# Performance work log

Measured on AMD Instinct MI355X. Metric: run time of the kernel, lower is better.

Reference implementation:

```python
import jax, jax.numpy as jnp
import numpy as np

WS = 8        # window_size
NH = 16       # num_heads
EPS = 1e-5    # BatchNorm eps (inference mode: running_mean=0, running_var=1)

def conv2d(x, w, padding=0, groups=1):
    return jax.lax.conv_general_dilated(
        x, w, (1, 1), [(padding, padding), (padding, padding)],
        dimension_numbers=('NCHW', 'OIHW', 'NCHW'), feature_group_count=groups)

def bn(x, gamma, beta):
    # eval-mode BatchNorm with running_mean=0, running_var=1
    return x * (gamma / jnp.sqrt(1.0 + EPS))[None, :, None, None] + beta[None, :, None, None]

def avgpool(x, kh, kw, ph, pw):
    # torch AvgPool2d with count_include_pad=True: sum over zero-padded window / (kh*kw)
    s = jax.lax.reduce_window(x, 0.0, jax.lax.add, (1, 1, kh, kw), (1, 1, 1, 1),
                              [(0, 0), (0, 0), (ph, ph), (pw, pw)])
    return s / float(kh * kw)

def rel_pos_index(ws):
    coords = np.stack(np.meshgrid(np.arange(ws), np.arange(ws), indexing='ij')).reshape(2, -1)
    rel = (coords[:, :, None] - coords[:, None, :]).transpose(1, 2, 0) + (ws - 1)
    return (rel[..., 0] * (2 * ws - 1) + rel[..., 1]).reshape(-1)

def hge_kernels(W):
    # build 4 directional Sobel kernels + Gaussian-Laplacian from learned scalars
    S0, S45, S90 = W[:, :, 0, 0], W[:, :, 0, 1], W[:, :, 0, 2]
    S135, GL = W[:, :, 1, 0], W[:, :, 2, 2]
    z = jnp.zeros_like(S0)
    k3 = lambda rows: jnp.stack([jnp.stack(r, -1) for r in rows], -2)  # [O,I,3,3]
    w0 = k3([[S0, 2*S0, S0], [z, z, z], [-S0, -2*S0, -S0]])
    w45 = k3([[2*S45, S45, z], [S45, z, -S45], [z, -S45, -2*S45]])
    w90 = k3([[S90, z, -S90], [2*S90, z, -2*S90], [S90, z, -S90]])
    w135 = k3([[z, -S135, -2*S135], [S135, z, -S135], [2*S135, S135, z]])
    a1 = GL * 4.0; a2 = -a1 / 8.0; a3 = -a1 / 16.0
    wGL = jnp.zeros(S0.shape + (5, 5), S0.dtype)
    for i, j, v in [(0,2,a3),(1,1,a3),(1,2,a2),(1,3,a3),(2,0,a3),(2,1,a2),(2,2,a1),
                    (2,3,a2),(2,4,a3),(3,1,a3),(3,2,a2),(3,3,a3),(4,2,a3)]:
        wGL = wGL.at[:, :, i, j].set(v)
    return w0, w45, w90, w135, wGL

def forward(x, ca_h1, ca_w1, ca_fh, ca_fw, l1_w, l1_g, l1_b, l2_w, l2_g, l2_b,
            hge_w, hge_fc_w, hge_fc_b, qkv_w, rel_table, proj_dw, proj_g, proj_b, proj_pw):
    B, C, H, W = x.shape
    d = C // NH
    scale = d ** -0.5
    # --- CA block: coordinate attention (1x1 convs on H- and W-pooled features) ---
    cm = lambda w, t: jnp.einsum('oc,bc...->bo...', w, t)
    s_h = jax.nn.sigmoid(cm(ca_fh, cm(ca_h1, x.mean(3))))   # [B,C,H]
    s_w = jax.nn.sigmoid(cm(ca_fw, cm(ca_w1, x.mean(2))))   # [B,C,W]
    x = x * s_h[:, :, :, None] * s_w[:, :, None, :]
    # --- local branch: 1x1 ConvBN + 3x3 ConvBN + HGE edge operator ---
    local = bn(conv2d(x, l2_w), l2_g, l2_b) + bn(conv2d(x, l1_w, padding=1), l1_g, l1_b)
    w0, w45, w90, w135, wGL = hge_kernels(hge_w)
    feats = jnp.concatenate([conv2d(x, w0, 1), conv2d(x, w45, 1), conv2d(x, w90, 1),
                             conv2d(x, w135, 1), conv2d(x, wGL, 2)], axis=1)  # [B,5C,H,W]
    local = local + conv2d(feats, hge_fc_w) + hge_fc_b[None, :, None, None]
    # --- windowed attention ---
    ph, pw = (-H) % WS, (-W) % WS
    if ph or pw:
        x = jnp.pad(x, ((0, 0), (0, 0), (0, ph), (0, pw)), mode='reflect')
    Hp, Wp = x.shape[2], x.shape[3]
    hh, ww = Hp // WS, Wp // WS
    qkv = conv2d(x, qkv_w)                                   # [B,3C,Hp,Wp]
    qkv = qkv.reshape(B, 3, NH, d, hh, WS, ww, WS)
    qkv = qkv.transpose(1, 0, 4, 6, 2, 5, 7, 3).reshape(3, B * hh * ww, NH, WS * WS, d)
    q, k, v = qkv[0], qkv[1], qkv[2]
    bias = rel_table[rel_pos_index(WS)].reshape(WS * WS, WS * WS, NH).transpose(2, 0, 1)
    dots = jnp.einsum('wnid,wnjd->wnij', q, k) * scale + bias[None]
    attn = jax.nn.softmax(dots, axis=-1)
    o = jnp.einsum('wnij,wnjd->wnid', attn, v)
    o = o.reshape(B, hh, ww, NH, WS, WS, d).transpose(0, 3, 6, 1, 4, 2, 5)
    o = o.reshape(B, C, Hp, Wp)[:, :, :H, :W]
    # --- directional average pooling of attention output ---
    ox = avgpool(jnp.pad(o, ((0, 0), (0, 0), (0, 1), (0, 0)), mode='reflect'), WS, 1, WS // 2 - 1, 0)
    oy = avgpool(jnp.pad(o, ((0, 0), (0, 0), (0, 0), (0, 1)), mode='reflect'), 1, WS, 0, WS // 2 - 1)
    out = ox + oy + local
    # --- pad_out + separable ConvBN projection (depthwise k=ws -> BN -> 1x1) ---
    out = jnp.pad(out, ((0, 0), (0, 0), (0, 1), (0, 1)), mode='reflect')
    out = conv2d(out, proj_dw, padding=(WS - 1) // 2, groups=C)
    out = bn(out, proj_g, proj_b)
    out = conv2d(out, proj_pw)
    return out[:, :, :H, :W]

def setup_inputs() -> dict:
    key = jax.random.key(0)
    ks = jax.random.split(key, 20)
    C = 128
    f32 = jnp.float32
    n = lambda k, sh, s: jax.random.normal(k, sh, f32) * s
    return {
        'x': jax.random.normal(ks[0], (2, C, 256, 256), f32),
        'ca_h1': n(ks[1], (C, C), 0.05), 'ca_w1': n(ks[2], (C, C), 0.05),
        'ca_fh': n(ks[3], (C, C), 0.05), 'ca_fw': n(ks[4], (C, C), 0.05),
        'l1_w': n(ks[5], (C, C, 3, 3), 0.03),
        'l1_g': 1.0 + n(ks[6], (C,), 0.02), 'l1_b': n(ks[7], (C,), 0.02),
        'l2_w': n(ks[8], (C, C, 1, 1), 0.09),
        'l2_g': 1.0 + n(ks[9], (C,), 0.02), 'l2_b': n(ks[10], (C,), 0.02),
        'hge_w': n(ks[11], (C, C, 3, 3), 0.02),
        'hge_fc_w': n(ks[12], (C, 5 * C, 1, 1), 0.02), 'hge_fc_b': n(ks[13], (C,), 0.02),
        'qkv_w': n(ks[14], (3 * C, C, 1, 1), 0.05),
        'rel_table': n(ks[15], ((2 * WS - 1) ** 2, NH), 0.02),
        'proj_dw': n(ks[16], (C, 1, WS, WS), 0.05),
        'proj_g': 1.0 + n(ks[17], (C,), 0.02), 'proj_b': n(ks[18], (C,), 0.02),
        'proj_pw': n(ks[19], (C, C, 1, 1), 0.05),
    }

def reference(x, ca_h1, ca_w1, ca_fh, ca_fw, l1_w, l1_g, l1_b, l2_w, l2_g, l2_b,
              hge_w, hge_fc_w, hge_fc_b, qkv_w, rel_table, proj_dw, proj_g, proj_b, proj_pw):
    return forward(x, ca_h1, ca_w1, ca_fh, ca_fw, l1_w, l1_g, l1_b, l2_w, l2_g, l2_b,
                   hge_w, hge_fc_w, hge_fc_b, qkv_w, rel_table, proj_dw, proj_g, proj_b, proj_pw)
```

## Files before the change

kernel.cpp:

```cpp
#include <hip/hip_runtime.h>

#define BB 2
#define CC 128
#define HWSZ 65536
#define RSQE 0.9999950000374997f
#define ATT_SCALE 0.35355339059327373f

typedef unsigned short u16;
using short8 = __attribute__((ext_vector_type(8))) short;
using f32x4  = __attribute__((ext_vector_type(4))) float;

#if defined(__has_builtin)
# if __has_builtin(__builtin_amdgcn_fdot2_f32_bf16)
#  define HAVE_DOT2 1
# endif
#endif

__device__ __forceinline__ float b2f(u16 u){
  return __uint_as_float(((unsigned int)u) << 16);
}
__device__ __forceinline__ u16 f2b(float f){
  unsigned int v = __float_as_uint(f);
  unsigned int r = (v + 0x7FFFu + ((v >> 16) & 1u)) >> 16;
  return (u16)r;
}

__device__ const int c_DI[13] = {-2,-1,-1,-1, 0, 0,0,0,0, 1,1,1, 2};
__device__ const int c_DJ[13] = { 0,-1, 0, 1,-2,-1,0,1,2,-1,0,1, 0};

__global__ void k_detect(const u16* __restrict__ xr, int* __restrict__ flag){
  __shared__ int ws_[4];
  int tid = threadIdx.x;
  int cnt = 0;
  for (int i = 0; i < 16; ++i){
    u16 u = xr[tid*16 + i];
    int e = (u >> 7) & 0xFF;
    cnt += (e < 100 || e > 141) ? 1 : 0;
  }
  #pragma unroll
  for (int off = 32; off > 0; off >>= 1) cnt += __shfl_down(cnt, off, 64);
  if ((tid & 63) == 0) ws_[tid >> 6] = cnt;
  __syncthreads();
  if (tid == 0) *flag = (ws_[0]+ws_[1]+ws_[2]+ws_[3] > 64) ? 1 : 0;
}

__global__ void k_ingest4(const void* __restrict__ src, u16* __restrict__ dst,
                          int n4, const int* __restrict__ flag){
  int i = blockIdx.x * 256 + threadIdx.x;
  if (i >= n4) return;
  if (*flag){
    float4 f = ((const float4*)src)[i];
    ushort4 r; r.x=f2b(f.x); r.y=f2b(f.y); r.z=f2b(f.z); r.w=f2b(f.w);
    ((ushort4*)dst)[i] = r;
  } else {
    ((ushort4*)dst)[i] = ((const ushort4*)src)[i];
  }
}

struct PtrL { const void* p[19]; };

__global__ void k_ingest_w(PtrL pl, u16* __restrict__ dst, const int* __restrict__ flag){
  const int ends[19] = {16384,32768,49152,65536,212992,213120,213248,229632,229760,
                        229888,377344,459264,459392,508544,512144,520336,520464,520592,536976};
  int g = blockIdx.x * 256 + threadIdx.x;
  int idx = g * 4;
  if (idx >= 536976) return;
  int seg = 0, start = 0;
  #pragma unroll
  for (int s = 0; s < 19; ++s){ if (idx >= ends[s]){ seg = s+1; start = ends[s]; } }
  int local = idx - start;
  const void* sp = pl.p[seg];
  if (*flag){
    float4 f = ((const float4*)sp)[local >> 2];
    ushort4 r; r.x=f2b(f.x); r.y=f2b(f.y); r.z=f2b(f.z); r.w=f2b(f.w);
    *(ushort4*)(dst + idx) = r;
  } else {
    *(ushort4*)(dst + idx) = ((const ushort4*)sp)[local >> 2];
  }
}

__global__ void k_prep_A(const u16* __restrict__ fh, const u16* __restrict__ h1,
                         const u16* __restrict__ fw, const u16* __restrict__ w1,
                         const u16* __restrict__ l1b, const u16* __restrict__ l2b,
                         const u16* __restrict__ fcb,
                         float* __restrict__ A_h, float* __restrict__ A_w,
                         float* __restrict__ biasK){
  int idx = blockIdx.x * 256 + threadIdx.x;
  int o = idx >> 7, c = idx & 127;
  float ah = 0.f, aw = 0.f;
  for (int m = 0; m < 128; ++m){
    ah += b2f(fh[o*128 + m]) * b2f(h1[m*128 + c]);
    aw += b2f(fw[o*128 + m]) * b2f(w1[m*128 + c]);
  }
  A_h[idx] = ah; A_w[idx] = aw;
  if (c == 0) biasK[o] = b2f(l1b[o]) + b2f(l2b[o]) + b2f(fcb[o]);
}

__global__ void k_prep_rel(const u16* __restrict__ rel, float* __restrict__ relo){
  int idx = blockIdx.x * 256 + threadIdx.x;
  if (idx >= 3600) return;
  int head = idx / 225, i = idx - head*225;
  relo[idx] = b2f(rel[i*16 + head]);
}

__global__ void k_prep_K(const u16* __restrict__ hge_w, const u16* __restrict__ fc_w,
                         const u16* __restrict__ l1_w, const u16* __restrict__ l1_g,
                         const u16* __restrict__ l2_w, const u16* __restrict__ l2_g,
                         u16* __restrict__ Kwb){
  int idx = blockIdx.x * 256 + threadIdx.x;
  int o = idx >> 7, c = idx & 127;
  float m0=0.f, m45=0.f, m90=0.f, m135=0.f, mgl=0.f;
  const u16* fo = fc_w + o*640;
  for (int m = 0; m < 128; ++m){
    const u16* hw9 = hge_w + (size_t)(m*128 + c)*9;
    m0   += b2f(fo[m      ]) * b2f(hw9[0]);
    m45  += b2f(fo[128 + m]) * b2f(hw9[1]);
    m90  += b2f(fo[256 + m]) * b2f(hw9[2]);
    m135 += b2f(fo[384 + m]) * b2f(hw9[3]);
    mgl  += b2f(fo[512 + m]) * b2f(hw9[8]);
  }
  float g1 = b2f(l1_g[o]) * RSQE;
  float g2 = b2f(l2_g[o]) * RSQE;
  float l1v[9];
  #pragma unroll
  for (int t = 0; t < 9; ++t) l1v[t] = b2f(l1_w[(size_t)idx*9 + t]) * g1;
  float l2v = b2f(l2_w[idx]) * g2;
  float kp[13];
  kp[0]  = -0.25f*mgl;
  kp[1]  =  m0 + 2.f*m45 + m90              - 0.25f*mgl + l1v[0];
  kp[2]  =  2.f*m0 + m45 - m135             - 0.50f*mgl + l1v[1];
  kp[3]  =  m0 - m90 - 2.f*m135             - 0.25f*mgl + l1v[2];
  kp[4]  = -0.25f*mgl;
  kp[5]  =  m45 + 2.f*m90 + m135            - 0.50f*mgl + l1v[3];
  kp[6]  =  4.f*mgl + l1v[4] + l2v;
  kp[7]  = -m45 - 2.f*m90 - m135            - 0.50f*mgl + l1v[5];
  kp[8]  = -0.25f*mgl;
  kp[9]  = -m0 + m90 + 2.f*m135             - 0.25f*mgl + l1v[6];
  kp[10] = -2.f*m0 - m45 + m135             - 0.50f*mgl + l1v[7];
  kp[11] = -m0 - 2.f*m45 - m90              - 0.25f*mgl + l1v[8];
  kp[12] = -0.25f*mgl;
  #pragma unroll
  for (int t = 0; t < 13; ++t) Kwb[t*16384 + idx] = f2b(kp[t]);
}

__global__ void k_means(const u16* __restrict__ x, float* __restrict__ mh, float* __restrict__ mw){
  __shared__ float colpart[4][256];
  int c = blockIdx.x, b = blockIdx.y;
  const u16* xp = x + (size_t)(b*CC + c)*HWSZ;
  int tid = threadIdx.x, lane = tid & 63, wv = tid >> 6;
  float c0=0.f,c1=0.f,c2=0.f,c3=0.f;
  for (int r = 0; r < 64; ++r){
    int h = wv*64 + r;
    ushort4 u = *(const ushort4*)(xp + h*256 + lane*4);
    float v0=b2f(u.x), v1=b2f(u.y), v2=b2f(u.z), v3=b2f(u.w);
    c0+=v0; c1+=v1; c2+=v2; c3+=v3;
    float rs = v0+v1+v2+v3;
    #pragma unroll
    for (int off = 32; off > 0; off >>= 1) rs += __shfl_down(rs, off, 64);
    if (lane == 0) mh[(size_t)(b*CC + c)*256 + h] = rs * (1.0f/256.0f);
  }
  colpart[wv][lane*4+0]=c0; colpart[wv][lane*4+1]=c1;
  colpart[wv][lane*4+2]=c2; colpart[wv][lane*4+3]=c3;
  __syncthreads();
  mw[(size_t)(b*CC + c)*256 + tid] =
    (colpart[0][tid]+colpart[1][tid]+colpart[2][tid]+colpart[3][tid]) * (1.0f/256.0f);
}

__global__ void k_sig(const float* __restrict__ A_h, const float* __restrict__ A_w,
                      const float* __restrict__ mh, const float* __restrict__ mw,
                      float* __restrict__ s_h, float* __restrict__ s_w){
  int o = blockIdx.x, b = blockIdx.y, sel = blockIdx.z, t = threadIdx.x;
  const float* A = sel ? A_w : A_h;
  const float* m = sel ? mw : mh;
  float* s = sel ? s_w : s_h;
  float acc = 0.f;
  for (int c = 0; c < 128; ++c)
    acc += A[o*128 + c] * m[(size_t)(b*CC + c)*256 + t];
  s[(size_t)(b*CC + o)*256 + t] = 1.0f / (1.0f + __expf(-acc));
}

__global__ void k_scale2cl(const u16* __restrict__ cx, const float* __restrict__ s_h,
                           const float* __restrict__ s_w, u16* __restrict__ xcl){
  __shared__ u16 t[16][136];
  int b = blockIdx.z >> 8, h = blockIdx.z & 255;
  int w0 = blockIdx.x * 16;
  int tid = threadIdx.x;
  int ic = tid >> 1, wseg = (tid & 1) * 8;
  uint4 v = *(const uint4*)(cx + (size_t)(b*CC + ic)*HWSZ + h*256 + w0 + wseg);
  float sh = s_h[(size_t)(b*CC + ic)*256 + h];
  const float* swp = s_w + (size_t)(b*CC + ic)*256 + w0 + wseg;
  float4 swa = *(const float4*)swp;
  float4 swb = *(const float4*)(swp + 4);
  u16 tmp[8]; *(uint4*)tmp = v;
  t[wseg+0][ic] = f2b(b2f(tmp[0])*sh*swa.x);
  t[wseg+1][ic] = f2b(b2f(tmp[1])*sh*swa.y);
  t[wseg+2][ic] = f2b(b2f(tmp[2])*sh*swa.z);
  t[wseg+3][ic] = f2b(b2f(tmp[3])*sh*swa.w);
  t[wseg+4][ic] = f2b(b2f(tmp[4])*sh*swb.x);
  t[wseg+5][ic] = f2b(b2f(tmp[5])*sh*swb.y);
  t[wseg+6][ic] = f2b(b2f(tmp[6])*sh*swb.z);
  t[wseg+7][ic] = f2b(b2f(tmp[7])*sh*swb.w);
  __syncthreads();
  int w = tid >> 4, part = (tid & 15) * 8;
  uint4 o = *(const uint4*)&t[w][part];
  *(uint4*)(xcl + ((size_t)(b*256 + h)*256 + (w0 + w))*128 + part) = o;
}

__global__ void k_cf2cl(const u16* __restrict__ src, u16* __restrict__ dst){
  __shared__ u16 t[16][136];
  int b = blockIdx.z >> 8, h = blockIdx.z & 255;
  int w0 = blockIdx.x * 16;
  int tid = threadIdx.x;
  int ic = tid >> 1, wseg = (tid & 1) * 8;
  uint4 v = *(const uint4*)(src + (size_t)(b*CC + ic)*HWSZ + h*256 + w0 + wseg);
  u16 tmp[8]; *(uint4*)tmp = v;
  #pragma unroll
  for (int k = 0; k < 8; ++k) t[wseg + k][ic] = tmp[k];
  __syncthreads();
  int w = tid >> 4, part = (tid & 15) * 8;
  uint4 o = *(const uint4*)&t[w][part];
  *(uint4*)(dst + ((size_t)(b*256 + h)*256 + (w0 + w))*128 + part) = o;
}

__launch_bounds__(256)
__global__ void k_conv5m(const u16* __restrict__ xcl, const u16* __restrict__ Kwb,
                         const float* __restrict__ biasK, u16* __restrict__ outp){
  __shared__ u16 As[128][40];
  __shared__ u16 Bs[128][40];
  int tid = threadIdx.x;
  int wv = tid >> 6, lane = tid & 63;
  int q = lane >> 4, l16 = lane & 15;
  int pt = blockIdx.x;
  int b = pt >> 9, h = (pt >> 1) & 255, w0 = (pt & 1) << 7;
  int mrow = (wv & 1) << 6, nrow = (wv >> 1) << 6;
  int sr = tid >> 2, sp = (tid & 3) << 3;
  const u16* xb_b = xcl + (size_t)b*HWSZ*128;
  f32x4 acc[4][4];
  #pragma unroll
  for (int mt = 0; mt < 4; ++mt)
    #pragma unroll
    for (int nt = 0; nt < 4; ++nt) acc[mt][nt] = (f32x4){0.f,0.f,0.f,0.f};

  for (int kc = 0; kc < 52; ++kc){
    int t = kc >> 2, c0 = (kc & 3) << 5;
    int di = c_DI[t], dj = c_DJ[t];
    int hh2 = h + di;
    bool rowok = (unsigned)hh2 < 256u;
    const u16* rowp = xb_b + (size_t)(rowok ? hh2 : 0)*256*128 + c0 + sp;
    int col0 = w0 + dj + sr;
    int col1 = col0 + 64;
    __syncthreads();
    {
      uint4 va0 = {0,0,0,0}, va1 = {0,0,0,0};
      if (rowok && (unsigned)col0 < 256u) va0 = *(const uint4*)(rowp + col0*128);
      if (rowok && (unsigned)col1 < 256u) va1 = *(const uint4*)(rowp + col1*128);
      *(uint4*)&As[sr][sp] = va0;
      *(uint4*)&As[sr + 64][sp] = va1;
      const u16* Bb = Kwb + t*16384 + c0;
      *(uint4*)&Bs[sr][sp] = *(const uint4*)(Bb + sr*128 + sp);
      *(uint4*)&Bs[sr + 64][sp] = *(const uint4*)(Bb + (sr + 64)*128 + sp);
    }
    __syncthreads();
    short8 af[4], bf[4];
    #pragma unroll
    for (int mt = 0; mt < 4; ++mt) af[mt] = *(const short8*)&As[mrow + mt*16 + l16][q*8];
    #pragma unroll
    for (int nt = 0; nt < 4; ++nt) bf[nt] = *(const short8*)&Bs[nrow + nt*16 + l16][q*8];
    #pragma unroll
    for (int mt = 0; mt < 4; ++mt)
      #pragma unroll
      for (int nt = 0; nt < 4; ++nt)
        acc[mt][nt] = __builtin_amdgcn_mfma_f32_16x16x32_bf16(af[mt], bf[nt], acc[mt][nt], 0, 0, 0);
  }
  #pragma unroll
  for (int nt = 0; nt < 4; ++nt){
    int n = nrow + nt*16 + l16;
    float bv = biasK[n];
    size_t cbase = (size_t)(b*CC + n)*HWSZ + h*256 + w0;
    #pragma unroll
    for (int mt = 0; mt < 4; ++mt){
      int m = mrow + mt*16 + q*4;
      ushort4 st;
      st.x = f2b(acc[mt][nt][0] + bv);
      st.y = f2b(acc[mt][nt][1] + bv);
      st.z = f2b(acc[mt][nt][2] + bv);
      st.w = f2b(acc[mt][nt][3] + bv);
      *(ushort4*)(outp + cbase + m) = st;
    }
  }
}

__launch_bounds__(256)
__global__ void k_mgemm(const u16* __restrict__ Xcl, const u16* __restrict__ W,
                        u16* __restrict__ Y, float* __restrict__ Yf,
                        const int* __restrict__ flag, int nsel, int mode){
  __shared__ u16 As[128][136];
  __shared__ u16 Bs[128][136];
  int tid = threadIdx.x;
  int wv = tid >> 6, lane = tid & 63;
  int q = lane >> 4, l16 = lane & 15;
  int pt = blockIdx.x;
  int b = pt >> 9, h = (pt >> 1) & 255, w0 = (pt & 1) << 7;
  int mrow = (wv & 1) << 6, nrow = (wv >> 1) << 6;
  const u16* Abase = Xcl + ((size_t)(b*256 + h)*256 + w0)*128;
  #pragma unroll
  for (int i = 0; i < 8; ++i){
    int seg = i*256 + tid;
    *(uint4*)&As[seg >> 4][(seg & 15) << 3] = *(const uint4*)(Abase + seg*8);
  }
  for (int sel = 0; sel < nsel; ++sel){
    __syncthreads();
    const u16* Wb = W + sel*16384;
    #pragma unroll
    for (int i = 0; i < 8; ++i){
      int seg = i*256 + tid;
      *(uint4*)&Bs[seg >> 4][(seg & 15) << 3] = *(const uint4*)(Wb + seg*8);
    }
    __syncthreads();
    f32x4 acc[4][4];
    #pragma unroll
    for (int mt = 0; mt < 4; ++mt)
      #pragma unroll
      for (int nt = 0; nt < 4; ++nt) acc[mt][nt] = (f32x4){0.f,0.f,0.f,0.f};
    #pragma unroll
    for (int kc = 0; kc < 4; ++kc){
      short8 af[4], bf[4];
      #pragma unroll
      for (int mt = 0; mt < 4; ++mt) af[mt] = *(const short8*)&As[mrow + mt*16 + l16][kc*32 + q*8];
      #pragma unroll
      for (int nt = 0; nt < 4; ++nt) bf[nt] = *(const short8*)&Bs[nrow + nt*16 + l16][kc*32 + q*8];
      #pragma unroll
      for (int mt = 0; mt < 4; ++mt)
        #pragma unroll
        for (int nt = 0; nt < 4; ++nt)
          acc[mt][nt] = __builtin_amdgcn_mfma_f32_16x16x32_bf16(af[mt], bf[nt], acc[mt][nt], 0, 0, 0);
    }
    if (mode == 0){
      __syncthreads();
      #pragma unroll
      for (int mt = 0; mt < 4; ++mt){
        int m0i = mrow + mt*16 + q*4;
        #pragma unroll
        for (int nt = 0; nt < 4; ++nt){
          int n = nrow + nt*16 + l16;
          Bs[m0i+0][n] = f2b(acc[mt][nt][0]);
          Bs[m0i+1][n] = f2b(acc[mt][nt][1]);
          Bs[m0i+2][n] = f2b(acc[mt][nt][2]);
          Bs[m0i+3][n] = f2b(acc[mt][nt][3]);
        }
      }
      __syncthreads();
      int win = tid >> 4, head = tid & 15;
      size_t obase = (((((size_t)b*32 + (h >> 3))*32 + (w0 >> 3) + win)*3 + sel)*16 + head)*512
                     + (size_t)(h & 7)*64;
      #pragma unroll
      for (int pj = 0; pj < 8; ++pj){
        uint4 vv = *(const uint4*)&Bs[win*8 + pj][head*8];
        *(uint4*)(Y + obase + pj*8) = vv;
      }
    } else {
      int f32o = (Yf != nullptr) && (*flag != 0);
      #pragma unroll
      for (int nt = 0; nt < 4; ++nt){
        int n = nrow + nt*16 + l16;
        size_t cbase = (size_t)(b*CC + n)*HWSZ + h*256 + w0;
        #pragma unroll
        for (int mt = 0; mt < 4; ++mt){
          int m = mrow + mt*16 + q*4;
          if (f32o){
            float4 st; st.x=acc[mt][nt][0]; st.y=acc[mt][nt][1];
            st.z=acc[mt][nt][2]; st.w=acc[mt][nt][3];
            *(float4*)(Yf + cbase + m) = st;
          } else {
            ushort4 st;
            st.x = f2b(acc[mt][nt][0]); st.y = f2b(acc[mt][nt][1]);
            st.z = f2b(acc[mt][nt][2]); st.w = f2b(acc[mt][nt][3]);
            *(ushort4*)(Y + cbase + m) = st;
          }
        }
      }
    }
  }
}

__launch_bounds__(256)
__global__ void k_attn3(const u16* __restrict__ qkvw, const float* __restrict__ relo,
                        u16* __restrict__ obuf){
  __shared__ float relf[228];
  __shared__ u16  kls[4][64][8];
  __shared__ float vls[4][64][8];
  int tid = threadIdx.x, wv = tid >> 6, lane = tid & 63;
  int b = blockIdx.z >> 4, head = blockIdx.z & 15;
  int hh = blockIdx.y, ww = blockIdx.x * 4 + wv;

  for (int e = tid; e < 225; e += 256) relf[e] = relo[head*225 + e];

  size_t base = (((size_t)b*32 + hh)*32 + ww)*3*8192 + (size_t)head*512;
  uint4 qv = *(const uint4*)(qkvw + base + lane*8);
  *(uint4*)&kls[wv][lane][0] = *(const uint4*)(qkvw + base + 8192 + lane*8);
  {
    uint4 raw = *(const uint4*)(qkvw + base + 16384 + lane*8);
    u16 tv[8]; *(uint4*)tv = raw;
    float4 lo, hi;
    lo.x=b2f(tv[0]); lo.y=b2f(tv[1]); lo.z=b2f(tv[2]); lo.w=b2f(tv[3]);
    hi.x=b2f(tv[4]); hi.y=b2f(tv[5]); hi.z=b2f(tv[6]); hi.w=b2f(tv[7]);
    *(float4*)&vls[wv][lane][0] = lo;
    *(float4*)&vls[wv][lane][4] = hi;
  }
  __syncthreads();

  int qi = lane >> 3, qj = lane & 7;
  const float* rbase = relf + (qi + 7)*15 + (qj + 7);
  float s[64];
#if HAVE_DOT2
  typedef __bf16 bf2 __attribute__((ext_vector_type(2)));
  bf2 q0 = __builtin_bit_cast(bf2, qv.x), q1 = __builtin_bit_cast(bf2, qv.y);
  bf2 q2 = __builtin_bit_cast(bf2, qv.z), q3 = __builtin_bit_cast(bf2, qv.w);
  #pragma unroll
  for (int kp = 0; kp < 64; ++kp){
    uint4 kv = *(const uint4*)&kls[wv][kp][0];
    float d = __builtin_amdgcn_fdot2_f32_bf16(q3, __builtin_bit_cast(bf2, kv.w), 0.f, false);
    d = __builtin_amdgcn_fdot2_f32_bf16(q2, __builtin_bit_cast(bf2, kv.z), d, false);
    d = __builtin_amdgcn_fdot2_f32_bf16(q1, __builtin_bit_cast(bf2, kv.y), d, false);
    d = __builtin_amdgcn_fdot2_f32_bf16(q0, __builtin_bit_cast(bf2, kv.x), d, false);
    s[kp] = fmaf(d, ATT_SCALE, rbase[-((kp>>3)*15 + (kp&7))]);
  }
#else
  float qf[8];
  { u16 tq[8]; *(uint4*)tq = qv;
    #pragma unroll
    for (int d = 0; d < 8; ++d) qf[d] = b2f(tq[d]); }
  #pragma unroll
  for (int kp = 0; kp < 64; ++kp){
    uint4 kv = *(const uint4*)&kls[wv][kp][0];
    u16 tk[8]; *(uint4*)tk = kv;
    float d = 0.f;
    #pragma unroll
    for (int dd = 0; dd < 8; ++dd) d = fmaf(qf[dd], b2f(tk[dd]), d);
    s[kp] = fmaf(d, ATT_SCALE, rbase[-((kp>>3)*15 + (kp&7))]);
  }
#endif
  float t16[16];
  #pragma unroll
  for (int i = 0; i < 16; ++i)
    t16[i] = fmaxf(fmaxf(s[i], s[i+16]), fmaxf(s[i+32], s[i+48]));
  float mx = t16[0];
  #pragma unroll
  for (int i = 1; i < 16; ++i) mx = fmaxf(mx, t16[i]);
  #pragma unroll
  for (int kp = 0; kp < 64; ++kp) s[kp] = __expf(s[kp] - mx);
  #pragma unroll
  for (int i = 0; i < 16; ++i)
    t16[i] = (s[i] + s[i+16]) + (s[i+32] + s[i+48]);
  float sum = t16[0];
  #pragma unroll
  for (int i = 1; i < 16; ++i) sum += t16[i];
  float inv = 1.0f / sum;
  float ov[8] = {0.f,0.f,0.f,0.f,0.f,0.f,0.f,0.f};
  #pragma unroll
  for (int kp = 0; kp < 64; ++kp){
    float4 va = *(const float4*)&vls[wv][kp][0];
    float4 vb = *(const float4*)&vls[wv][kp][4];
    float pp = s[kp];
    ov[0] = fmaf(pp, va.x, ov[0]); ov[1] = fmaf(pp, va.y, ov[1]);
    ov[2] = fmaf(pp, va.z, ov[2]); ov[3] = fmaf(pp, va.w, ov[3]);
    ov[4] = fmaf(pp, vb.x, ov[4]); ov[5] = fmaf(pp, vb.y, ov[5]);
    ov[6] = fmaf(pp, vb.z, ov[6]); ov[7] = fmaf(pp, vb.w, ov[7]);
  }
  size_t obase = (size_t)(b*CC + head*8)*HWSZ + (size_t)(hh*8 + qi)*256 + ww*8 + qj;
  #pragma unroll
  for (int d = 0; d < 8; ++d)
    obuf[obase + (size_t)d*HWSZ] = f2b(ov[d] * inv);
}

__launch_bounds__(256)
__global__ void k_pool2(const u16* __restrict__ obuf, u16* __restrict__ localb){
  __shared__ u16 t[71][88];
  int bc = blockIdx.z;
  int h0 = blockIdx.y * 64, w0 = blockIdx.x * 64;
  int tid = threadIdx.x;
  const u16* op = obuf + (size_t)bc * HWSZ;

  for (int e = tid; e < 710; e += 256){
    int tr = e / 10, ci = e - tr*10;
    int gt = h0 - 3 + tr;
    if (gt == 256) gt = 254;
    bool rv = (unsigned)gt <= 255u;
    int g0 = w0 - 8 + ci*8;
    uint4 v = {0,0,0,0};
    if (rv){
      if (g0 >= 0 && g0 <= 248){
        v = *(const uint4*)(op + gt*256 + g0);
      } else {
        u16 tmp[8];
        #pragma unroll
        for (int j = 0; j < 8; ++j){
          int g = g0 + j;
          if (g == 256) g = 254;
          tmp[j] = ((unsigned)g <= 255u) ? op[gt*256 + g] : (u16)0;
        }
        v = *(const uint4*)tmp;
      }
    }
    *(uint4*)&t[tr][ci*8] = v;
  }
  __syncthreads();

  int ty = tid >> 4, tx = tid & 15;
  int r0 = ty*4, c0 = tx*4;
  float sxv[4][4];
  #pragma unroll
  for (int c = 0; c < 4; ++c){
    float col[11];
    #pragma unroll
    for (int i = 0; i < 11; ++i) col[i] = b2f(t[r0+i][c0+8+c]);
    float s = ((col[0]+col[1])+(col[2]+col[3]))+((col[4]+col[5])+(col[6]+col[7]));
    sxv[0][c] = s;
    s += col[8]  - col[0]; sxv[1][c] = s;
    s += col[9]  - col[1]; sxv[2][c] = s;
    s += col[10] - col[2]; sxv[3][c] = s;
  }
  #pragma unroll
  for (int r = 0; r < 4; ++r){
    int rr = r0 + r;
    float pre[11];
    #pragma unroll
    for (int j = 0; j < 11; ++j) pre[j] = b2f(t[rr+3][c0+5+j]);
    float sy0 = ((pre[0]+pre[1])+(pre[2]+pre[3]))+((pre[4]+pre[5])+(pre[6]+pre[7]));
    float sy1 = sy0 + pre[8]  - pre[0];
    float sy2 = sy1 + pre[9]  - pre[1];
    float sy3 = sy2 + pre[10] - pre[2];
    size_t base = (size_t)bc*HWSZ + (size_t)(h0+rr)*256 + (w0+c0);
    ushort4 lv = *(const ushort4*)(localb + base);
    ushort4 st;
    st.x = f2b((sxv[r][0]+sy0)*0.125f + b2f(lv.x));
    st.y = f2b((sxv[r][1]+sy1)*0.125f + b2f(lv.y));
    st.z = f2b((sxv[r][2]+sy2)*0.125f + b2f(lv.z));
    st.w = f2b((sxv[r][3]+sy3)*0.125f + b2f(lv.w));
    *(ushort4*)(localb + base) = st;
  }
}

__launch_bounds__(256)
__global__ void k_dw2(const u16* __restrict__ u_, const u16* __restrict__ dww,
                      const u16* __restrict__ g, const u16* __restrict__ bta,
                      u16* __restrict__ dwout){
  __shared__ u16 xt[71][152];
  int c = blockIdx.z & 127, b = blockIdx.z >> 7;
  int h0 = blockIdx.y * 64, w0 = blockIdx.x * 128;
  int tid = threadIdx.x;
  const u16* up = u_ + (size_t)(b*CC + c)*HWSZ;

  for (int e = tid; e < 71*18; e += 256){
    int tr = e / 18, ci = e - tr*18;
    int gt = h0 - 3 + tr;
    if (gt == 256) gt = 254;
    int g0 = w0 - 8 + ci*8;
    uint4 v = {0,0,0,0};
    if ((unsigned)gt <= 255u){
      if (g0 >= 0 && g0 <= 248){
        v = *(const uint4*)(up + gt*256 + g0);
      } else {
        u16 tmp[8];
        #pragma unroll
        for (int j = 0; j < 8; ++j){
          int gw = g0 + j;
          if (gw == 256) gw = 254;
          tmp[j] = ((unsigned)gw <= 255u) ? up[gt*256 + gw] : (u16)0;
        }
        v = *(const uint4*)tmp;
      }
    }
    *(uint4*)&xt[tr][ci*8] = v;
  }

#if HAVE_DOT2
  typedef __bf16 bf2v __attribute__((ext_vector_type(2)));
  unsigned int wp[32];
  {
    const uint4* wsrc = (const uint4*)(dww + c*64);
    #pragma unroll
    for (int t = 0; t < 8; ++t){
      uint4 v = wsrc[t];
      wp[t*4+0]=v.x; wp[t*4+1]=v.y; wp[t*4+2]=v.z; wp[t*4+3]=v.w;
    }
  }
#else
  float wf[64];
  {
    const u16* wsrc = dww + c*64;
    #pragma unroll
    for (int t = 0; t < 64; ++t) wf[t] = b2f(wsrc[t]);
  }
#endif
  __syncthreads();

  int tx = tid & 15, ty = tid >> 4;
  int r0 = ty*4;
  int cb = tx*8;
  float acc[4][8];
  #pragma unroll
  for (int r = 0; r < 4; ++r)
    #pragma unroll
    for (int k = 0; k < 8; ++k) acc[r][k] = 0.f;

  #pragma unroll
  for (int i = 0; i < 11; ++i){
    const u16* rowp = &xt[r0 + i][cb + 4];
    uint2 av = *(const uint2*)(rowp);
    uint4 mv = *(const uint4*)(rowp + 4);
    uint2 zv = *(const uint2*)(rowp + 12);
    unsigned int d0=av.x, d1=av.y, d2=mv.x, d3=mv.y, d4=mv.z, d5=mv.w, d6=zv.x, d7=zv.y;
    unsigned int dd[8] = {d0,d1,d2,d3,d4,d5,d6,d7};
#if HAVE_DOT2
    unsigned int xp[15];
    #pragma unroll
    for (int t = 1; t < 15; ++t)
      xp[t] = (t & 1) ? ((dd[t>>1] >> 16) | (dd[(t>>1)+1] << 16)) : dd[t>>1];
    #pragma unroll
    for (int dr = 0; dr < 4; ++dr){
      int wr = i - dr;
      if (wr >= 0 && wr < 8){
        #pragma unroll
        for (int k = 0; k < 8; ++k){
          float s = acc[dr][k];
          #pragma unroll
          for (int p = 0; p < 4; ++p)
            s = __builtin_amdgcn_fdot2_f32_bf16(
                  __builtin_bit_cast(bf2v, wp[wr*4+p]),
                  __builtin_bit_cast(bf2v, xp[1+k+2*p]), s, false);
          acc[dr][k] = s;
        }
      }
    }
#else
    float xw[16];
    #pragma unroll
    for (int t = 1; t < 16; ++t){
      unsigned int w32 = dd[t>>1];
      xw[t] = __uint_as_float((t & 1) ? (w32 & 0xFFFF0000u) : (w32 << 16));
    }
    #pragma unroll
    for (int dr = 0; dr < 4; ++dr){
      int wr = i - dr;
      if (wr >= 0 && wr < 8){
        #pragma unroll
        for (int k = 0; k < 8; ++k){
          float s = acc[dr][k];
          #pragma unroll
          for (int j = 0; j < 8; ++j)
            s = fmaf(wf[wr*8+j], xw[1+k+j], s);
          acc[dr][k] = s;
        }
      }
    }
#endif
  }

  float scale = b2f(g[c]) * RSQE;
  float bb = b2f(bta[c]);
  size_t obase = (size_t)(b*CC + c)*HWSZ + (size_t)(h0 + r0)*256 + w0 + cb;
  #pragma unroll
  for (int r = 0; r < 4; ++r){
    u16 po[8];
    #pragma unroll
    for (int k = 0; k < 8; ++k) po[k] = f2b(acc[r][k]*scale + bb);
    *(uint4*)(dwout + obase + (size_t)r*256) = *(uint4*)po;
  }
}

extern "C" void kernel_launch(void* const* d_in, const int* in_sizes, int n_in,
                              void* d_out, int out_size, void* d_ws, size_t ws_size,
                              hipStream_t stream) {
  char* p = (char*)d_ws;
  u16* cx     = (u16*)p; p += 33554432;
  u16* xcl    = (u16*)p; p += 33554432;
  u16* qkvb   = (u16*)p; p += 100663296;
  u16* cw     = (u16*)p; p += 1074176;
  float* A_h    = (float*)p; p += 65536;
  float* A_w    = (float*)p; p += 65536;
  u16*  Kwb     = (u16*)p;  p += 425984;
  float* biasK  = (float*)p; p += 1024;
  float* mh     = (float*)p; p += 262144;
  float* mw     = (float*)p; p += 262144;
  float* s_h    = (float*)p; p += 262144;
  float* s_w    = (float*)p; p += 262144;
  int* flag     = (int*)p;   p += 256;
  float* relo   = (float*)p; p += 16384;

  u16* localb = (u16*)d_out;
  u16* qkvw   = qkvb;
  u16* obuf   = cx;
  u16* dwbuf  = qkvb;
  u16* dwcl   = xcl;

  const int O_h1=0, O_w1=16384, O_fh=32768, O_fw=49152, O_l1w=65536, O_l1g=212992,
            O_l1b=213120, O_l2w=213248, O_l2g=229632, O_l2b=229760, O_hge=229888,
            O_fcw=377344, O_fcb=459264, O_qkvw=459392, O_rel=508544, O_dw=512144,
            O_pg=520336, O_pb=520464, O_pw=520592;

  k_detect<<<1, 256, 0, stream>>>((const u16*)d_in[0], flag);
  k_ingest4<<<16384, 256, 0, stream>>>(d_in[0], cx, 4194304, flag);
  PtrL pl;
  for (int i = 0; i < 19; ++i) pl.p[i] = d_in[i+1];
  k_ingest_w<<<525, 256, 0, stream>>>(pl, cw, flag);

  k_prep_A<<<64, 256, 0, stream>>>(cw+O_fh, cw+O_h1, cw+O_fw, cw+O_w1,
                                   cw+O_l1b, cw+O_l2b, cw+O_fcb, A_h, A_w, biasK);
  k_prep_rel<<<15, 256, 0, stream>>>(cw+O_rel, relo);
  k_prep_K<<<64, 256, 0, stream>>>(cw+O_hge, cw+O_fcw, cw+O_l1w, cw+O_l1g,
                                   cw+O_l2w, cw+O_l2g, Kwb);
  k_means<<<dim3(128, 2), 256, 0, stream>>>(cx, mh, mw);
  k_sig<<<dim3(128, 2, 2), 256, 0, stream>>>(A_h, A_w, mh, mw, s_h, s_w);
  k_scale2cl<<<dim3(16, 1, 512), 256, 0, stream>>>(cx, s_h, s_w, xcl);

  k_conv5m<<<1024, 256, 0, stream>>>(xcl, Kwb, biasK, localb);
  k_mgemm<<<1024, 256, 0, stream>>>(xcl, cw+O_qkvw, qkvw, nullptr, flag, 3, 0);
  k_attn3<<<dim3(8, 32, 32), 256, 0, stream>>>(qkvw, relo, obuf);
  k_pool2<<<dim3(4, 4, 256), 256, 0, stream>>>(obuf, localb);
  k_dw2<<<dim3(2, 4, 256), 256, 0, stream>>>(localb, cw+O_dw, cw+O_pg, cw+O_pb, dwbuf);
  k_cf2cl<<<dim3(16, 1, 512), 256, 0, stream>>>(dwbuf, dwcl);
  k_mgemm<<<1024, 256, 0, stream>>>(dwcl, cw+O_pw, (u16*)d_out, (float*)d_out, flag, 1, 1);
}
```

Before: 572.0 us.

## Restructure 5x5 sparse conv to stage one input row per kernel row and reuse across taps

The conv kernel now loads a full halo-padded input row (132 pixels x 128 channels) into shared memory once per kernel row and reuses it for every horizontal tap in that row, instead of restaging the input for each of the 13 taps. Weight fragments are read straight from global memory rather than staged in LDS, and block indices are remapped so that consecutive blocks touch different image rows, which changes cache locality. This cuts global input traffic and the number of barriers, at the cost of uncoalesced global weight loads in the inner loop and more LDS per block, which may lower occupancy.

```diff
diff --git a/kernel.cpp b/kernel.cpp
--- a/kernel.cpp
+++ b/kernel.cpp
@@ -24,9 +24,6 @@
   unsigned int r = (v + 0x7FFFu + ((v >> 16) & 1u)) >> 16;
   return (u16)r;
 }
-
-__device__ const int c_DI[13] = {-2,-1,-1,-1, 0, 0,0,0,0, 1,1,1, 2};
-__device__ const int c_DJ[13] = { 0,-1, 0, 1,-2,-1,0,1,2,-1,0,1, 0};
 
 __global__ void k_detect(const u16* __restrict__ xr, int* __restrict__ flag){
   __shared__ int ws_[4];
@@ -223,17 +220,16 @@
 }
 
 __launch_bounds__(256)
-__global__ void k_conv5m(const u16* __restrict__ xcl, const u16* __restrict__ Kwb,
+__global__ void k_conv5r(const u16* __restrict__ xcl, const u16* __restrict__ Kwb,
                          const float* __restrict__ biasK, u16* __restrict__ outp){
-  __shared__ u16 As[128][40];
-  __shared__ u16 Bs[128][40];
+  __shared__ u16 As[132][136];
   int tid = threadIdx.x;
   int wv = tid >> 6, lane = tid & 63;
   int q = lane >> 4, l16 = lane & 15;
-  int pt = blockIdx.x;
+  int pt0 = blockIdx.x;
+  int pt = (pt0 & 7) * 128 + (pt0 >> 3);
   int b = pt >> 9, h = (pt >> 1) & 255, w0 = (pt & 1) << 7;
   int mrow = (wv & 1) << 6, nrow = (wv >> 1) << 6;
-  int sr = tid >> 2, sp = (tid & 3) << 3;
   const u16* xb_b = xcl + (size_t)b*HWSZ*128;
   f32x4 acc[4][4];
   #pragma unroll
@@ -241,36 +237,47 @@
     #pragma unroll
     for (int nt = 0; nt < 4; ++nt) acc[mt][nt] = (f32x4){0.f,0.f,0.f,0.f};
 
-  for (int kc = 0; kc < 52; ++kc){
-    int t = kc >> 2, c0 = (kc & 3) << 5;
-    int di = c_DI[t], dj = c_DJ[t];
-    int hh2 = h + di;
+  const int rowTap0[5] = {0,1,4,9,12};
+  const int rowNTap[5] = {1,3,5,3,1};
+  const int rowDj0[5]  = {0,-1,-2,-1,0};
+
+  for (int ri = 0; ri < 5; ++ri){
+    int hh2 = h + ri - 2;
     bool rowok = (unsigned)hh2 < 256u;
-    const u16* rowp = xb_b + (size_t)(rowok ? hh2 : 0)*256*128 + c0 + sp;
-    int col0 = w0 + dj + sr;
-    int col1 = col0 + 64;
     __syncthreads();
     {
-      uint4 va0 = {0,0,0,0}, va1 = {0,0,0,0};
-      if (rowok && (unsigned)col0 < 256u) va0 = *(const uint4*)(rowp + col0*128);
-      if (rowok && (unsigned)col1 < 256u) va1 = *(const uint4*)(rowp + col1*128);
-      *(uint4*)&As[sr][sp] = va0;
-      *(uint4*)&As[sr + 64][sp] = va1;
-      const u16* Bb = Kwb + t*16384 + c0;
-      *(uint4*)&Bs[sr][sp] = *(const uint4*)(Bb + sr*128 + sp);
-      *(uint4*)&Bs[sr + 64][sp] = *(const uint4*)(Bb + (sr + 64)*128 + sp);
+      const u16* rowbase = xb_b + (size_t)(rowok ? hh2 : 0)*256*128;
+      for (int e = tid; e < 2112; e += 256){
+        int px = e >> 4, chunk = (e & 15) << 3;
+        int col = w0 - 2 + px;
+        uint4 v = {0,0,0,0};
+        if (rowok && (unsigned)col < 256u)
+          v = *(const uint4*)(rowbase + col*128 + chunk);
+        *(uint4*)&As[px][chunk] = v;
+      }
     }
     __syncthreads();
-    short8 af[4], bf[4];
-    #pragma unroll
-    for (int mt = 0; mt < 4; ++mt) af[mt] = *(const short8*)&As[mrow + mt*16 + l16][q*8];
-    #pragma unroll
-    for (int nt = 0; nt < 4; ++nt) bf[nt] = *(const short8*)&Bs[nrow + nt*16 + l16][q*8];
-    #pragma unroll
-    for (int mt = 0; mt < 4; ++mt)
+    int ntap = rowNTap[ri];
+    for (int tt = 0; tt < ntap; ++tt){
+      int t = rowTap0[ri] + tt;
+      int dj = rowDj0[ri] + tt;
+      const u16* Bb = Kwb + t*16384;
       #pragma unroll
-      for (int nt = 0; nt < 4; ++nt)
-        acc[mt][nt] = __builtin_amdgcn_mfma_f32_16x16x32_bf16(af[mt], bf[nt], acc[mt][nt], 0, 0, 0);
+      for (int kc = 0; kc < 4; ++kc){
+        short8 af[4], bf[4];
+        #pragma unroll
+        for (int mt = 0; mt < 4; ++mt)
+          af[mt] = *(const short8*)&As[mrow + mt*16 + l16 + dj + 2][kc*32 + q*8];
+        #pragma unroll
+        for (int nt = 0; nt < 4; ++nt)
+          bf[nt] = *(const short8*)(Bb + (nrow + nt*16 + l16)*128 + kc*32 + q*8);
+        #pragma unroll
+        for (int mt = 0; mt < 4; ++mt)
+          #pragma unroll
+          for (int nt = 0; nt < 4; ++nt)
+            acc[mt][nt] = __builtin_amdgcn_mfma_f32_16x16x32_bf16(af[mt], bf[nt], acc[mt][nt], 0, 0, 0);
+      }
+    }
   }
   #pragma unroll
   for (int nt = 0; nt < 4; ++nt){
@@ -714,7 +721,7 @@
   k_sig<<<dim3(128, 2, 2), 256, 0, stream>>>(A_h, A_w, mh, mw, s_h, s_w);
   k_scale2cl<<<dim3(16, 1, 512), 256, 0, stream>>>(cx, s_h, s_w, xcl);
 
-  k_conv5m<<<1024, 256, 0, stream>>>(xcl, Kwb, biasK, localb);
+  k_conv5r<<<1024, 256, 0, stream>>>(xcl, Kwb, biasK, localb);
   k_mgemm<<<1024, 256, 0, stream>>>(xcl, cw+O_qkvw, qkvw, nullptr, flag, 3, 0);
   k_attn3<<<dim3(8, 32, 32), 256, 0, stream>>>(qkvw, relo, obuf);
   k_pool2<<<dim3(4, 4, 256), 256, 0, stream>>>(obuf, localb);
```

Result: slower. 599.1 us (+4.7%).
